# Kernel optimization log

Hardware: AMD Instinct MI355X
Metric: run time of the kernel (lower is better)

## Reference

```python
import jax, jax.numpy as jnp
import numpy as np

EPS = 1e-16

def setup_inputs() -> dict:
    B, N, M, D = 32, 16384, 128, 1024
    L = 3 * M + 6  # write_lengths sum: k(M), beta(1), g(1), s(3), gamma(1), e(M), a(M)
    ks = jax.random.split(jax.random.key(0), 5)
    embeddings = jax.random.normal(ks[0], (B, D), jnp.float32)
    w_prev = jax.random.uniform(ks[1], (B, N), jnp.float32)
    w_prev = w_prev / jnp.sum(w_prev, axis=1, keepdims=True)  # valid address distribution
    mem = jax.random.normal(ks[2], (B, N, M), jnp.float32) * 0.05
    # Dense params: variance_scaling(1.4, fan_avg, uniform) ~ U(-lim, lim)
    lim = float(np.sqrt(3.0 * 1.4 / ((D + L) / 2.0)))
    W = jax.random.uniform(ks[3], (D, L), jnp.float32, -lim, lim)
    b = jax.random.normal(ks[4], (L,), jnp.float32) * 0.01
    return {"embeddings": embeddings, "w_prev": w_prev, "mem": mem, "W": W, "b": b}

def _forward(embeddings, w_prev, mem, W, b):
    M = mem.shape[-1]
    o = embeddings @ W + b  # [B, 3M+6]
    k = o[:, :M]
    beta = jax.nn.softplus(o[:, M:M + 1])
    g = jax.nn.sigmoid(o[:, M + 1:M + 2])
    s = jax.nn.softmax(o[:, M + 2:M + 5], axis=1)  # 3-tap shift
    gamma = 1.0 + jax.nn.softplus(o[:, M + 5:M + 6])
    e = jax.nn.sigmoid(o[:, M + 6:2 * M + 6])
    a = o[:, 2 * M + 6:]
    # content addressing: cosine similarity -> softmax(beta * sim)
    sim = jnp.einsum('bnm,bm->bn', mem, k) / (
        jnp.linalg.norm(mem, axis=-1) * jnp.linalg.norm(k, axis=-1, keepdims=True) + EPS)
    w_c = jax.nn.softmax(beta * sim, axis=1)
    # interpolation with previous weights
    w_g = g * w_c + (1.0 - g) * w_prev
    # circular convolution with 3-tap shift kernel s = [s(-1), s(0), s(+1)]
    w_t = (s[:, 0:1] * jnp.roll(w_g, 1, axis=1)
           + s[:, 1:2] * w_g
           + s[:, 2:3] * jnp.roll(w_g, -1, axis=1))
    # sharpening
    w_sh = w_t ** gamma
    w = w_sh / (jnp.sum(w_sh, axis=1, keepdims=True) + EPS)
    # erase + add write: mem' = mem * (1 - w e^T) + w a^T
    we = w[:, :, None] * e[:, None, :]  # [B, N, M]
    wa = w[:, :, None] * a[:, None, :]
    new_mem = mem * (1.0 - we) + wa
    return w, new_mem

def reference(embeddings, w_prev, mem, W, b):
    return _forward(embeddings, w_prev, mem, W, b)
```

## Files before the change

### kernel.cpp

```cpp
#include <hip/hip_runtime.h>
#include <math.h>

#define B 32
#define N 16384
#define M 128
#define D 1024
#define L 390
#define EPSF 1e-16f

#define O_OFF  0
#define P_OFF  (B*L)
#define S1_OFF (P_OFF + B*8)
#define S2_OFF (S1_OFF + B)
#define Z_OFF  (S2_OFF + B)

typedef float fvec4 __attribute__((ext_vector_type(4)));

__device__ __forceinline__ float softplusf(float x) {
    return x > 20.f ? x : log1pf(expf(x));
}
__device__ __forceinline__ float sigmoidf(float x) {
    return 1.f / (1.f + expf(-x));
}

__global__ __launch_bounds__(256) void k1_gemm(const float* __restrict__ emb,
                                               const float* __restrict__ W,
                                               const float* __restrict__ bias,
                                               float* __restrict__ ws) {
    __shared__ float embS[D];
    __shared__ float red[4][64];
    const int l0 = blockIdx.x * 64;
    const int b  = blockIdx.y;
    const int t  = threadIdx.x;
    for (int i = t; i < D; i += 256) embS[i] = emb[b * D + i];
    __syncthreads();
    const int li = t & 63;
    const int q  = t >> 6;
    const int l  = l0 + li;
    float partial = 0.f;
    if (l < L) {
        const float* wp = W + (size_t)(q * 256) * L + l;
        #pragma unroll 8
        for (int d = 0; d < 256; ++d) partial += embS[q * 256 + d] * wp[(size_t)d * L];
    }
    red[q][li] = partial;
    __syncthreads();
    if (t < 64 && l0 + t < L) {
        float o = red[0][t] + red[1][t] + red[2][t] + red[3][t] + bias[l0 + t];
        ws[O_OFF + b * L + l0 + t] = o;
    }
}

__global__ __launch_bounds__(128) void k1b_act(float* __restrict__ ws) {
    const int b = blockIdx.x;
    const int t = threadIdx.x;
    const float* o = ws + O_OFF + b * L;
    float kv = o[t];
    float sq = kv * kv;
    #pragma unroll
    for (int off = 32; off >= 1; off >>= 1) sq += __shfl_xor(sq, off, 64);
    __shared__ float s01[2];
    if ((t & 63) == 0) s01[t >> 6] = sq;
    __syncthreads();
    if (t == 0) {
        float knorm = sqrtf(s01[0] + s01[1]);
        float beta  = softplusf(o[M]);
        float g     = sigmoidf(o[M + 1]);
        float x0 = o[M + 2], x1 = o[M + 3], x2 = o[M + 4];
        float mx = fmaxf(x0, fmaxf(x1, x2));
        float e0 = expf(x0 - mx), e1 = expf(x1 - mx), e2 = expf(x2 - mx);
        float inv = 1.f / (e0 + e1 + e2);
        float gamma = 1.f + softplusf(o[M + 5]);
        float* p = ws + P_OFF + b * 8;
        p[0] = beta; p[1] = g; p[2] = e0 * inv; p[3] = e1 * inv; p[4] = e2 * inv;
        p[5] = gamma; p[6] = knorm;
        ws[S1_OFF + b] = 0.f;
        ws[S2_OFF + b] = 0.f;
    }
}

__global__ __launch_bounds__(256) void k2_sim(const float* __restrict__ mem,
                                              float* __restrict__ ws) {
    const int b    = blockIdx.y;
    const int n0   = blockIdx.x * 64;
    const int t    = threadIdx.x;
    const int wave = t >> 6, lane = t & 63;
    __shared__ float kS[M];
    if (t < M) kS[t] = ws[O_OFF + b * L + t];
    __syncthreads();
    const float beta  = ws[P_OFF + b * 8 + 0];
    const float knorm = ws[P_OFF + b * 8 + 6];
    float* z = ws + Z_OFF + (size_t)b * N;
    const int seg = (lane & 15) * 8;
    const float4 ka = *(const float4*)&kS[seg];
    const float4 kb = *(const float4*)&kS[seg + 4];
    float lsum = 0.f;
    #pragma unroll
    for (int it = 0; it < 4; ++it) {
        const int n = n0 + wave * 16 + it * 4 + (lane >> 4);
        const float* mp = mem + ((size_t)b * N + n) * M + seg;
        const float4 ma = *(const float4*)mp;
        const float4 mb = *(const float4*)(mp + 4);
        float dot = ma.x*ka.x + ma.y*ka.y + ma.z*ka.z + ma.w*ka.w
                  + mb.x*kb.x + mb.y*kb.y + mb.z*kb.z + mb.w*kb.w;
        float sq  = ma.x*ma.x + ma.y*ma.y + ma.z*ma.z + ma.w*ma.w
                  + mb.x*mb.x + mb.y*mb.y + mb.z*mb.z + mb.w*mb.w;
        #pragma unroll
        for (int off = 1; off <= 8; off <<= 1) {
            dot += __shfl_xor(dot, off, 64);
            sq  += __shfl_xor(sq,  off, 64);
        }
        if ((lane & 15) == 0) {
            const float sim = dot / (sqrtf(sq) * knorm + EPSF);
            const float u   = expf(beta * sim);
            z[n] = u;
            lsum += u;
        }
    }
    lsum += __shfl_xor(lsum, 16, 64);
    lsum += __shfl_xor(lsum, 32, 64);
    __shared__ float acc[4];
    if (lane == 0) acc[wave] = lsum;
    __syncthreads();
    if (t == 0) atomicAdd(ws + S1_OFF + b, acc[0] + acc[1] + acc[2] + acc[3]);
}

__global__ __launch_bounds__(256) void k3_shsum(const float* __restrict__ w_prev,
                                                float* __restrict__ ws,
                                                float* __restrict__ out) {
    const int b = blockIdx.y;
    const int n = blockIdx.x * 256 + threadIdx.x;
    const float* p = ws + P_OFF + b * 8;
    const float g = p[1], s0 = p[2], s1 = p[3], s2 = p[4], gamma = p[5];
    const float invS1 = 1.f / ws[S1_OFF + b];
    const float* u  = ws + Z_OFF + (size_t)b * N;
    const float* wp = w_prev + (size_t)b * N;
    const int nm = (n == 0)     ? N - 1 : n - 1;
    const int np = (n == N - 1) ? 0     : n + 1;
    const float gm1 = 1.f - g;
    const float gi  = g * invS1;
    const float wgm = gi * u[nm] + gm1 * wp[nm];
    const float wg0 = gi * u[n ] + gm1 * wp[n ];
    const float wgp = gi * u[np] + gm1 * wp[np];
    const float wt  = s0 * wgm + s1 * wg0 + s2 * wgp;
    const float v = powf(wt, gamma);
    out[(size_t)b * N + n] = v;
    float r = v;
    #pragma unroll
    for (int off = 32; off >= 1; off >>= 1) r += __shfl_xor(r, off, 64);
    __shared__ float acc[4];
    if ((threadIdx.x & 63) == 0) acc[threadIdx.x >> 6] = r;
    __syncthreads();
    if (threadIdx.x == 0) atomicAdd(ws + S2_OFF + b, acc[0] + acc[1] + acc[2] + acc[3]);
}

__global__ __launch_bounds__(256) void k4_write(const float* __restrict__ mem,
                                                const float* __restrict__ ws,
                                                float* __restrict__ out) {
    const int b    = blockIdx.y;
    const int n0   = (gridDim.x - 1 - blockIdx.x) * 64;
    const int t    = threadIdx.x;
    const int wave = t >> 6, lane = t & 63;
    __shared__ float eS[M], aS[M];
    if (t < M) {
        eS[t] = sigmoidf(ws[O_OFF + b * L + M + 6 + t]);
        aS[t] = ws[O_OFF + b * L + 2 * M + 6 + t];
    }
    __syncthreads();
    const float invS2 = 1.f / (ws[S2_OFF + b] + EPSF);
    float* w_out = out + (size_t)b * N;
    float* m_out = out + (size_t)B * N;
    const int col = (lane & 31) * 4;
    const fvec4 ev = *(const fvec4*)&eS[col];
    const fvec4 av = *(const fvec4*)&aS[col];
    #pragma unroll
    for (int it = 0; it < 8; ++it) {
        const int n = n0 + wave * 16 + it * 2 + (lane >> 5);
        const float wsh = w_out[n];
        const float wv  = wsh * invS2;
        const size_t idx = ((size_t)b * N + n) * M + col;
        const fvec4 mv = *(const fvec4*)(mem + idx);
        fvec4 r;
        r.x = fmaf(mv.x, fmaf(-wv, ev.x, 1.f), wv * av.x);
        r.y = fmaf(mv.y, fmaf(-wv, ev.y, 1.f), wv * av.y);
        r.z = fmaf(mv.z, fmaf(-wv, ev.z, 1.f), wv * av.z);
        r.w = fmaf(mv.w, fmaf(-wv, ev.w, 1.f), wv * av.w);
        __builtin_nontemporal_store(r, (fvec4*)(m_out + idx));
        if ((lane & 31) == 0)
            __builtin_nontemporal_store(wv, w_out + n);
    }
}

extern "C" void kernel_launch(void* const* d_in, const int* in_sizes, int n_in,
                              void* d_out, int out_size, void* d_ws, size_t ws_size,
                              hipStream_t stream) {
    const float* emb    = (const float*)d_in[0];
    const float* w_prev = (const float*)d_in[1];
    const float* mem    = (const float*)d_in[2];
    const float* W      = (const float*)d_in[3];
    const float* bias   = (const float*)d_in[4];
    float* ws  = (float*)d_ws;
    float* out = (float*)d_out;

    k1_gemm <<<dim3(7, B),      256, 0, stream>>>(emb, W, bias, ws);
    k1b_act <<<dim3(B),         128, 0, stream>>>(ws);
    k2_sim  <<<dim3(N / 64, B), 256, 0, stream>>>(mem, ws);
    k3_shsum<<<dim3(N / 256, B),256, 0, stream>>>(w_prev, ws, out);
    k4_write<<<dim3(N / 64, B), 256, 0, stream>>>(mem, ws, out);
}
```

Measured before the change: 561.7 us.

## Fuse all stages into one cooperative persistent kernel with grid syncs

Replaces the five separate launches (projection GEMM, activations, similarity, shift/sharpen sum, memory write) with one cooperative kernel of 1024 blocks. Each block owns a fixed chunk of rows of one batch, and the stages are separated by grid-wide syncs. This removes launch gaps and keeps each block on the same memory rows for the similarity read and the write pass, which may give cache reuse. In exchange, the projection GEMM now runs on only 32 blocks, each thread doing a serial 1024-long dot product, and the reversed block order that the old write kernel used for cache reuse is dropped. The old kernels remain as a fallback if the cooperative launch fails.

After: 971.9 us. 1.73x slower.

```diff
diff --git a/kernel.cpp b/kernel.cpp
--- a/kernel.cpp
+++ b/kernel.cpp
@@ -1,5 +1,8 @@
 #include <hip/hip_runtime.h>
+#include <hip/hip_cooperative_groups.h>
 #include <math.h>
+
+namespace cg = cooperative_groups;
 
 #define B 32
 #define N 16384
@@ -8,6 +11,10 @@
 #define L 390
 #define EPSF 1e-16f
 
+#define GRID  1024
+#define BPB   (GRID / B)
+#define CHUNK (N / BPB)
+
 #define O_OFF  0
 #define P_OFF  (B*L)
 #define S1_OFF (P_OFF + B*8)
@@ -21,6 +28,160 @@
 }
 __device__ __forceinline__ float sigmoidf(float x) {
     return 1.f / (1.f + expf(-x));
+}
+
+__global__ __launch_bounds__(256, 4) void fused_all(
+    const float* __restrict__ emb, const float* __restrict__ w_prev,
+    const float* __restrict__ mem, const float* __restrict__ Wm,
+    const float* __restrict__ bias, float* __restrict__ ws,
+    float* __restrict__ out)
+{
+    cg::grid_group gg = cg::this_grid();
+    __shared__ float sm[D];
+    __shared__ float oS[L];
+    __shared__ float sred[8];
+    const int t    = threadIdx.x;
+    const int blk  = blockIdx.x;
+    const int wave = t >> 6, lane = t & 63;
+
+    if (blk < B) {
+        const int b = blk;
+        for (int i = t; i < D; i += 256) sm[i] = emb[b * D + i];
+        __syncthreads();
+        for (int l = t; l < L; l += 256) {
+            float acc = 0.f;
+            const float* wp = Wm + l;
+            #pragma unroll 8
+            for (int d = 0; d < D; ++d) acc = fmaf(sm[d], wp[(size_t)d * L], acc);
+            acc += bias[l];
+            ws[O_OFF + b * L + l] = acc;
+            oS[l] = acc;
+        }
+        __syncthreads();
+        if (t < 128) {
+            float kv = oS[t];
+            float sq = kv * kv;
+            #pragma unroll
+            for (int off = 32; off >= 1; off >>= 1) sq += __shfl_xor(sq, off, 64);
+            if ((t & 63) == 0) sred[t >> 6] = sq;
+        }
+        __syncthreads();
+        if (t == 0) {
+            float knorm = sqrtf(sred[0] + sred[1]);
+            float beta  = softplusf(oS[M]);
+            float g     = sigmoidf(oS[M + 1]);
+            float x0 = oS[M + 2], x1 = oS[M + 3], x2 = oS[M + 4];
+            float mx = fmaxf(x0, fmaxf(x1, x2));
+            float e0 = expf(x0 - mx), e1 = expf(x1 - mx), e2 = expf(x2 - mx);
+            float inv = 1.f / (e0 + e1 + e2);
+            float gamma = 1.f + softplusf(oS[M + 5]);
+            float* p = ws + P_OFF + b * 8;
+            p[0] = beta; p[1] = g; p[2] = e0 * inv; p[3] = e1 * inv; p[4] = e2 * inv;
+            p[5] = gamma; p[6] = knorm;
+            ws[S1_OFF + b] = 0.f;
+            ws[S2_OFF + b] = 0.f;
+        }
+    }
+    gg.sync();
+
+    const int b  = blk / BPB;
+    const int n0 = (blk % BPB) * CHUNK;
+    float* u = ws + Z_OFF + (size_t)b * N;
+
+    if (t < M) sm[t] = ws[O_OFF + b * L + t];
+    __syncthreads();
+    {
+        const float beta  = ws[P_OFF + b * 8 + 0];
+        const float knorm = ws[P_OFF + b * 8 + 6];
+        const int seg = (lane & 15) * 8;
+        const fvec4 ka = *(const fvec4*)&sm[seg];
+        const fvec4 kb = *(const fvec4*)&sm[seg + 4];
+        float lsum = 0.f;
+        #pragma unroll 4
+        for (int it = 0; it < CHUNK / 16; ++it) {
+            const int n = n0 + wave * (CHUNK / 4) + it * 4 + (lane >> 4);
+            const float* mp = mem + ((size_t)b * N + n) * M + seg;
+            const fvec4 ma = *(const fvec4*)mp;
+            const fvec4 mb = *(const fvec4*)(mp + 4);
+            float dot = ma.x*ka.x + ma.y*ka.y + ma.z*ka.z + ma.w*ka.w
+                      + mb.x*kb.x + mb.y*kb.y + mb.z*kb.z + mb.w*kb.w;
+            float sq  = ma.x*ma.x + ma.y*ma.y + ma.z*ma.z + ma.w*ma.w
+                      + mb.x*mb.x + mb.y*mb.y + mb.z*mb.z + mb.w*mb.w;
+            #pragma unroll
+            for (int off = 1; off <= 8; off <<= 1) {
+                dot += __shfl_xor(dot, off, 64);
+                sq  += __shfl_xor(sq,  off, 64);
+            }
+            if ((lane & 15) == 0) {
+                const float sim = dot / (sqrtf(sq) * knorm + EPSF);
+                const float uu  = expf(beta * sim);
+                u[n] = uu;
+                lsum += uu;
+            }
+        }
+        lsum += __shfl_xor(lsum, 16, 64);
+        lsum += __shfl_xor(lsum, 32, 64);
+        if (lane == 0) sred[wave] = lsum;
+        __syncthreads();
+        if (t == 0) atomicAdd(ws + S1_OFF + b, sred[0] + sred[1] + sred[2] + sred[3]);
+    }
+    gg.sync();
+
+    {
+        const float* p = ws + P_OFF + b * 8;
+        const float g = p[1], s0 = p[2], s1v = p[3], s2v = p[4], gamma = p[5];
+        const float invS1 = 1.f / ws[S1_OFF + b];
+        const float gi = g * invS1, gm1 = 1.f - g;
+        const float* wp = w_prev + (size_t)b * N;
+        float ls = 0.f;
+        #pragma unroll
+        for (int k2 = 0; k2 < CHUNK / 256; ++k2) {
+            const int n  = n0 + k2 * 256 + t;
+            const int nm = (n == 0)     ? N - 1 : n - 1;
+            const int np = (n == N - 1) ? 0     : n + 1;
+            const float wgm = gi * u[nm] + gm1 * wp[nm];
+            const float wg0 = gi * u[n ] + gm1 * wp[n ];
+            const float wgp = gi * u[np] + gm1 * wp[np];
+            const float wt  = s0 * wgm + s1v * wg0 + s2v * wgp;
+            const float v = powf(wt, gamma);
+            out[(size_t)b * N + n] = v;
+            ls += v;
+        }
+        #pragma unroll
+        for (int off = 32; off >= 1; off >>= 1) ls += __shfl_xor(ls, off, 64);
+        if (lane == 0) sred[4 + wave] = ls;
+        __syncthreads();
+        if (t == 0) atomicAdd(ws + S2_OFF + b, sred[4] + sred[5] + sred[6] + sred[7]);
+    }
+    gg.sync();
+
+    if (t < M) {
+        sm[t]     = sigmoidf(ws[O_OFF + b * L + M + 6 + t]);
+        sm[M + t] = ws[O_OFF + b * L + 2 * M + 6 + t];
+    }
+    __syncthreads();
+    {
+        const float invS2 = 1.f / (ws[S2_OFF + b] + EPSF);
+        float* w_out = out + (size_t)b * N;
+        float* m_out = out + (size_t)B * N;
+        const int col = (lane & 31) * 4;
+        const fvec4 ev = *(const fvec4*)&sm[col];
+        const fvec4 av = *(const fvec4*)&sm[M + col];
+        #pragma unroll 4
+        for (int it = 0; it < CHUNK / 8; ++it) {
+            const int n = n0 + wave * (CHUNK / 4) + it * 2 + (lane >> 5);
+            const float wv = w_out[n] * invS2;
+            const size_t idx = ((size_t)b * N + n) * M + col;
+            const fvec4 mv = *(const fvec4*)(mem + idx);
+            fvec4 r;
+            r.x = fmaf(mv.x, fmaf(-wv, ev.x, 1.f), wv * av.x);
+            r.y = fmaf(mv.y, fmaf(-wv, ev.y, 1.f), wv * av.y);
+            r.z = fmaf(mv.z, fmaf(-wv, ev.z, 1.f), wv * av.z);
+            r.w = fmaf(mv.w, fmaf(-wv, ev.w, 1.f), wv * av.w);
+            __builtin_nontemporal_store(r, (fvec4*)(m_out + idx));
+            if ((lane & 31) == 0) w_out[n] = wv;
+        }
+    }
 }
 
 __global__ __launch_bounds__(256) void k1_gemm(const float* __restrict__ emb,
@@ -112,9 +273,9 @@
         }
         if ((lane & 15) == 0) {
             const float sim = dot / (sqrtf(sq) * knorm + EPSF);
-            const float u   = expf(beta * sim);
-            z[n] = u;
-            lsum += u;
+            const float uu  = expf(beta * sim);
+            z[n] = uu;
+            lsum += uu;
         }
     }
     lsum += __shfl_xor(lsum, 16, 64);
@@ -202,9 +363,16 @@
     float* ws  = (float*)d_ws;
     float* out = (float*)d_out;
 
-    k1_gemm <<<dim3(7, B),      256, 0, stream>>>(emb, W, bias, ws);
-    k1b_act <<<dim3(B),         128, 0, stream>>>(ws);
-    k2_sim  <<<dim3(N / 64, B), 256, 0, stream>>>(mem, ws);
-    k3_shsum<<<dim3(N / 256, B),256, 0, stream>>>(w_prev, ws, out);
-    k4_write<<<dim3(N / 64, B), 256, 0, stream>>>(mem, ws, out);
-}
+    void* args[] = {(void*)&emb, (void*)&w_prev, (void*)&mem, (void*)&W,
+                    (void*)&bias, (void*)&ws, (void*)&out};
+    hipError_t err = hipLaunchCooperativeKernel((const void*)fused_all,
+                                                dim3(GRID), dim3(256),
+                                                args, 0, stream);
+    if (err != hipSuccess) {
+        k1_gemm <<<dim3(7, B),       256, 0, stream>>>(emb, W, bias, ws);
+        k1b_act <<<dim3(B),          128, 0, stream>>>(ws);
+        k2_sim  <<<dim3(N / 64, B),  256, 0, stream>>>(mem, ws);
+        k3_shsum<<<dim3(N / 256, B), 256, 0, stream>>>(w_prev, ws, out);
+        k4_write<<<dim3(N / 64, B),  256, 0, stream>>>(mem, ws, out);
+    }
+}
```

## Use one thread per memory row in similarity kernel; prefetch weights in write kernel

Applied to the files above, without the earlier changes.

The similarity kernel now gives each thread a whole 128-float memory row and loops over it with vector loads. This replaces the old scheme of 16 lanes per row followed by shuffle reductions, and the kernel launches 4x fewer blocks. The write kernel loads all eight normalized weights up front, reads memory with nontemporal loads, and writes the weights back after the main loop. The cost is that per-thread row traversal gives strided, poorly coalesced global loads, because neighbouring lanes are 512 bytes apart.

Measured after the change: 536.5 us. 1.05x faster.

```diff
diff --git a/kernel.cpp b/kernel.cpp
--- a/kernel.cpp
+++ b/kernel.cpp
@@ -81,46 +81,36 @@
 
 __global__ __launch_bounds__(256) void k2_sim(const float* __restrict__ mem,
                                               float* __restrict__ ws) {
-    const int b    = blockIdx.y;
-    const int n0   = blockIdx.x * 64;
-    const int t    = threadIdx.x;
+    const int b = blockIdx.y;
+    const int t = threadIdx.x;
+    const int n = blockIdx.x * 256 + t;
     const int wave = t >> 6, lane = t & 63;
     __shared__ float kS[M];
     if (t < M) kS[t] = ws[O_OFF + b * L + t];
     __syncthreads();
     const float beta  = ws[P_OFF + b * 8 + 0];
     const float knorm = ws[P_OFF + b * 8 + 6];
-    float* z = ws + Z_OFF + (size_t)b * N;
-    const int seg = (lane & 15) * 8;
-    const float4 ka = *(const float4*)&kS[seg];
-    const float4 kb = *(const float4*)&kS[seg + 4];
-    float lsum = 0.f;
-    #pragma unroll
-    for (int it = 0; it < 4; ++it) {
-        const int n = n0 + wave * 16 + it * 4 + (lane >> 4);
-        const float* mp = mem + ((size_t)b * N + n) * M + seg;
-        const float4 ma = *(const float4*)mp;
-        const float4 mb = *(const float4*)(mp + 4);
-        float dot = ma.x*ka.x + ma.y*ka.y + ma.z*ka.z + ma.w*ka.w
-                  + mb.x*kb.x + mb.y*kb.y + mb.z*kb.z + mb.w*kb.w;
-        float sq  = ma.x*ma.x + ma.y*ma.y + ma.z*ma.z + ma.w*ma.w
-                  + mb.x*mb.x + mb.y*mb.y + mb.z*mb.z + mb.w*mb.w;
-        #pragma unroll
-        for (int off = 1; off <= 8; off <<= 1) {
-            dot += __shfl_xor(dot, off, 64);
-            sq  += __shfl_xor(sq,  off, 64);
-        }
-        if ((lane & 15) == 0) {
-            const float sim = dot / (sqrtf(sq) * knorm + EPSF);
-            const float u   = expf(beta * sim);
-            z[n] = u;
-            lsum += u;
-        }
-    }
-    lsum += __shfl_xor(lsum, 16, 64);
-    lsum += __shfl_xor(lsum, 32, 64);
+    const float* mp = mem + ((size_t)b * N + n) * M;
+
+    float dot = 0.f, sq = 0.f;
+    #pragma unroll 16
+    for (int j = 0; j < M / 4; ++j) {
+        const fvec4 mv = *(const fvec4*)(mp + j * 4);
+        const fvec4 kv = *(const fvec4*)&kS[j * 4];
+        dot = fmaf(mv.x, kv.x, dot); dot = fmaf(mv.y, kv.y, dot);
+        dot = fmaf(mv.z, kv.z, dot); dot = fmaf(mv.w, kv.w, dot);
+        sq  = fmaf(mv.x, mv.x, sq);  sq  = fmaf(mv.y, mv.y, sq);
+        sq  = fmaf(mv.z, mv.z, sq);  sq  = fmaf(mv.w, mv.w, sq);
+    }
+    const float sim = dot / (sqrtf(sq) * knorm + EPSF);
+    const float uu  = expf(beta * sim);
+    ws[Z_OFF + (size_t)b * N + n] = uu;
+
+    float r = uu;
+    #pragma unroll
+    for (int off = 32; off >= 1; off >>= 1) r += __shfl_xor(r, off, 64);
     __shared__ float acc[4];
-    if (lane == 0) acc[wave] = lsum;
+    if (lane == 0) acc[wave] = r;
     __syncthreads();
     if (t == 0) atomicAdd(ws + S1_OFF + b, acc[0] + acc[1] + acc[2] + acc[3]);
 }
@@ -170,24 +160,35 @@
     const float invS2 = 1.f / (ws[S2_OFF + b] + EPSF);
     float* w_out = out + (size_t)b * N;
     float* m_out = out + (size_t)B * N;
-    const int col = (lane & 31) * 4;
+    const int col  = (lane & 31) * 4;
+    const int half = lane >> 5;
+    const int base = n0 + wave * 16;
     const fvec4 ev = *(const fvec4*)&eS[col];
     const fvec4 av = *(const fvec4*)&aS[col];
+
+    float wv[8];
+    #pragma unroll
+    for (int it = 0; it < 8; ++it)
+        wv[it] = w_out[base + it * 2 + half] * invS2;
+
     #pragma unroll
     for (int it = 0; it < 8; ++it) {
-        const int n = n0 + wave * 16 + it * 2 + (lane >> 5);
-        const float wsh = w_out[n];
-        const float wv  = wsh * invS2;
+        const int n = base + it * 2 + half;
         const size_t idx = ((size_t)b * N + n) * M + col;
-        const fvec4 mv = *(const fvec4*)(mem + idx);
+        const fvec4 mv = __builtin_nontemporal_load((const fvec4*)(mem + idx));
+        const float w = wv[it];
         fvec4 r;
-        r.x = fmaf(mv.x, fmaf(-wv, ev.x, 1.f), wv * av.x);
-        r.y = fmaf(mv.y, fmaf(-wv, ev.y, 1.f), wv * av.y);
-        r.z = fmaf(mv.z, fmaf(-wv, ev.z, 1.f), wv * av.z);
-        r.w = fmaf(mv.w, fmaf(-wv, ev.w, 1.f), wv * av.w);
+        r.x = fmaf(mv.x, fmaf(-w, ev.x, 1.f), w * av.x);
+        r.y = fmaf(mv.y, fmaf(-w, ev.y, 1.f), w * av.y);
+        r.z = fmaf(mv.z, fmaf(-w, ev.z, 1.f), w * av.z);
+        r.w = fmaf(mv.w, fmaf(-w, ev.w, 1.f), w * av.w);
         __builtin_nontemporal_store(r, (fvec4*)(m_out + idx));
-        if ((lane & 31) == 0)
-            __builtin_nontemporal_store(wv, w_out + n);
+    }
+
+    if ((lane & 31) == 0) {
+        #pragma unroll
+        for (int it = 0; it < 8; ++it)
+            w_out[base + it * 2 + half] = wv[it];
     }
 }
 
@@ -202,9 +203,9 @@
     float* ws  = (float*)d_ws;
     float* out = (float*)d_out;
 
-    k1_gemm <<<dim3(7, B),      256, 0, stream>>>(emb, W, bias, ws);
-    k1b_act <<<dim3(B),         128, 0, stream>>>(ws);
-    k2_sim  <<<dim3(N / 64, B), 256, 0, stream>>>(mem, ws);
-    k3_shsum<<<dim3(N / 256, B),256, 0, stream>>>(w_prev, ws, out);
-    k4_write<<<dim3(N / 64, B), 256, 0, stream>>>(mem, ws, out);
-}
+    k1_gemm <<<dim3(7, B),       256, 0, stream>>>(emb, W, bias, ws);
+    k1b_act <<<dim3(B),          128, 0, stream>>>(ws);
+    k2_sim  <<<dim3(N / 256, B), 256, 0, stream>>>(mem, ws);
+    k3_shsum<<<dim3(N / 256, B), 256, 0, stream>>>(w_prev, ws, out);
+    k4_write<<<dim3(N / 64, B),  256, 0, stream>>>(mem, ws, out);
+}
```
